# Kernel tuning notes

Measured on AMD Instinct MI355X. Metric: run time of the kernel, lower is better.

## Reference

```python
import jax, jax.numpy as jnp
import numpy as np

B, N, ND, ED, HD = 2, 384, 128, 32, 128
MSG_IN = 2 * ND + ED + 1  # 289
LN_EPS = 1e-3  # keras LayerNormalization default epsilon


def setup_inputs() -> dict:
    key = jax.random.key(0)
    ks = jax.random.split(key, 20)
    s = 0.05
    return {
        "h": jax.random.normal(ks[0], (B, N, ND), jnp.float32),
        "x": jax.random.normal(ks[1], (B, N, 3), jnp.float32),
        "edge_attr": jax.random.normal(ks[2], (B, N, N, ED), jnp.float32),
        "atom_mask": jnp.ones((B, N), jnp.float32),
        "msg_w1": jax.random.normal(ks[3], (MSG_IN, HD), jnp.float32) * s,
        "msg_b1": jnp.zeros((HD,), jnp.float32),
        "msg_w2": jax.random.normal(ks[4], (HD, HD), jnp.float32) * s,
        "msg_b2": jnp.zeros((HD,), jnp.float32),
        "node_w1": jax.random.normal(ks[5], (ND + HD, HD), jnp.float32) * s,
        "node_b1": jnp.zeros((HD,), jnp.float32),
        "node_w2": jax.random.normal(ks[6], (HD, ND), jnp.float32) * s,
        "node_b2": jnp.zeros((ND,), jnp.float32),
        "coord_w1": jax.random.normal(ks[7], (HD, HD), jnp.float32) * s,
        "coord_b1": jnp.zeros((HD,), jnp.float32),
        "coord_w2": jax.random.normal(ks[8], (HD, 1), jnp.float32) * 0.01,  # RandomNormal(0, 0.01)
        "ln_gamma": jnp.ones((ND,), jnp.float32),
        "ln_beta": jnp.zeros((ND,), jnp.float32),
        "adj": jax.random.randint(ks[9], (B, N, N), 0, 2, jnp.int32),
    }


def _layernorm(y, gamma, beta):
    mu = jnp.mean(y, axis=-1, keepdims=True)
    var = jnp.mean(jnp.square(y - mu), axis=-1, keepdims=True)
    return (y - mu) * jax.lax.rsqrt(var + LN_EPS) * gamma + beta


def reference(h, x, edge_attr, atom_mask,
              msg_w1, msg_b1, msg_w2, msg_b2,
              node_w1, node_b1, node_w2, node_b2,
              coord_w1, coord_b1, coord_w2,
              ln_gamma, ln_beta, adj):
    n = h.shape[1]
    rel_pos = x[:, :, None, :] - x[:, None, :, :]              # [B,N,N,3]
    dist_sq = jnp.sum(rel_pos ** 2, axis=-1, keepdims=True)    # [B,N,N,1]
    h_i = jnp.broadcast_to(h[:, :, None, :], (h.shape[0], n, n, h.shape[-1]))
    h_j = jnp.broadcast_to(h[:, None, :, :], (h.shape[0], n, n, h.shape[-1]))
    msg_in = jnp.concatenate([h_i, h_j, edge_attr, dist_sq], axis=-1)  # [B,N,N,289]
    m = jax.nn.silu(msg_in @ msg_w1 + msg_b1)
    m = jax.nn.silu(m @ msg_w2 + msg_b2)                        # [B,N,N,HD]
    adj_f = adj.astype(m.dtype)[..., None]                      # [B,N,N,1]
    m = m * adj_f
    h_agg = jnp.sum(m, axis=2)                                  # [B,N,HD]
    u = jax.nn.silu(jnp.concatenate([h, h_agg], axis=-1) @ node_w1 + node_b1)
    h_update = u @ node_w2 + node_b2
    h_new = _layernorm(h + h_update, ln_gamma, ln_beta)
    # coordinate update
    cw = jax.nn.silu(m @ coord_w1 + coord_b1) @ coord_w2        # [B,N,N,1]
    dist = jnp.sqrt(dist_sq + 1e-8)
    cw = cw / (dist + 1.0) * adj_f
    x_agg = jnp.sum(cw * rel_pos, axis=2) * atom_mask[..., None]
    x_new = x + x_agg
    return (h_new, x_new)
```

## Files before the change

### kernel.cpp

```cpp
#include <hip/hip_runtime.h>

typedef float f32x4 __attribute__((ext_vector_type(4)));
typedef unsigned int u32x4 __attribute__((ext_vector_type(4)));
typedef unsigned int u32x2 __attribute__((ext_vector_type(2)));
typedef __bf16 bf16x8 __attribute__((ext_vector_type(8)));

#define LDS_WET   0
#define LDS_W2T   10240
#define LDS_WC1T  45056
#define LDS_ACTW  79872
#define LDS_MBUFW 114688
#define LDS_FP    148480
#define LDS_CIDX  151552
#define LDS_WCNT  152320
#define LDS_BYTES 152388

__device__ __forceinline__ unsigned short f2bf(float f) {
  unsigned int u = __builtin_bit_cast(unsigned int, f);
  unsigned int r = u + 0x7FFFu + ((u >> 16) & 1u);
  return (unsigned short)(r >> 16);
}
__device__ __forceinline__ float bf2f(unsigned short hbits) {
  unsigned int u = ((unsigned int)hbits) << 16;
  return __builtin_bit_cast(float, u);
}
__device__ __forceinline__ unsigned int pk2(float lo, float hi) {
  return (unsigned int)f2bf(lo) | ((unsigned int)f2bf(hi) << 16);
}
__device__ __forceinline__ float silu_f(float xv) {
  float t = __builtin_amdgcn_exp2f(-1.44269504088896f * xv);
  return xv * __builtin_amdgcn_rcpf(1.0f + t);
}
__device__ __forceinline__ f32x4 mfma16(u32x4 a, u32x4 b, f32x4 c) {
  return __builtin_amdgcn_mfma_f32_16x16x32_bf16(
      __builtin_bit_cast(bf16x8, a), __builtin_bit_cast(bf16x8, b), c, 0, 0, 0);
}

__global__ void egnn_pre(const float* __restrict__ h,
                         const float* __restrict__ msg_w1,
                         const float* __restrict__ msg_b1,
                         float* __restrict__ his,
                         unsigned short* __restrict__ hjw) {
  __shared__ float hr[128];
  const int row = blockIdx.x;
  const int t = threadIdx.x;
  if (t < 128) hr[t] = h[(size_t)row*128 + t];
  __syncthreads();
  const int col = t & 127;
  const int base = (t < 128) ? 0 : 128;
  float s = (t < 128) ? msg_b1[col] : 0.0f;
  #pragma unroll 4
  for (int k = 0; k < 128; ++k) s += hr[k] * msg_w1[(size_t)(base + k)*128 + col];
  if (t < 128) his[(size_t)row*128 + col] = s;
  else         hjw[(size_t)row*128 + col] = f2bf(s);
}

__launch_bounds__(512, 1)
__global__ void egnn_main(
    const float* __restrict__ h, const float* __restrict__ x,
    const float* __restrict__ eattr, const float* __restrict__ amask,
    const float* __restrict__ msg_w1, const float* __restrict__ msg_w2,
    const float* __restrict__ msg_b2, const float* __restrict__ node_w1,
    const float* __restrict__ node_b1, const float* __restrict__ node_w2,
    const float* __restrict__ node_b2, const float* __restrict__ coord_w1,
    const float* __restrict__ coord_b1, const float* __restrict__ coord_w2,
    const float* __restrict__ ln_g, const float* __restrict__ ln_b,
    const int* __restrict__ adj, const float* __restrict__ his,
    const unsigned short* __restrict__ hjw, float* __restrict__ out)
{
  extern __shared__ char smem[];
  short* weT  = (short*)(smem + LDS_WET);
  short* w2T  = (short*)(smem + LDS_W2T);
  short* wc1T = (short*)(smem + LDS_WC1T);
  float* fp   = (float*)(smem + LDS_FP);
  float* HisL = fp;          float* wdL  = fp + 128;
  float* b2L  = fp + 256;    float* bc1L = fp + 384;
  float* wc2L = fp + 512;    float* hrow = fp + 640;
  unsigned short* cidx16 = (unsigned short*)(smem + LDS_CIDX);
  int* wcnt = (int*)(smem + LDS_WCNT);
  int* wsc  = wcnt + 8;

  const int tid  = threadIdx.x;
  const int bi   = blockIdx.x;
  const int bb   = (bi / 384) * 384;
  const int wave = tid >> 6;
  const int lane = tid & 63;
  const int g    = lane >> 4;
  const int lr   = lane & 15;
  short* actW = (short*)(smem + LDS_ACTW) + wave*16*136;
  short* mbW  = (short*)(smem + LDS_MBUFW) + wave*16*132;

  const bool pred = (tid < 384) && (adj[(size_t)bi*384 + tid] != 0);
  const unsigned long long bmask = __ballot(pred);
  if (lane == 0) wcnt[wave] = __popcll(bmask);

  for (int idx = tid; idx < 32*128; idx += 512) {
    int k = idx >> 7, d = idx & 127;
    weT[d*40 + k] = (short)f2bf(msg_w1[(size_t)(256 + k)*128 + d]);
  }
  for (int idx = tid; idx < 128*128; idx += 512) {
    int k = idx >> 7, d = idx & 127;
    w2T[d*136 + k]  = (short)f2bf(msg_w2[idx]);
    wc1T[d*136 + k] = (short)f2bf(coord_w1[idx]);
  }
  if (tid < 128) {
    HisL[tid] = his[(size_t)bi*128 + tid];
    wdL[tid]  = msg_w1[288*128 + tid];
    b2L[tid]  = msg_b2[tid];
    bc1L[tid] = coord_b1[tid];
    wc2L[tid] = coord_w2[tid];
    hrow[tid] = h[(size_t)bi*128 + tid];
  }
  __syncthreads();

  if (tid == 0) {
    int run = 0;
    #pragma unroll
    for (int w = 0; w < 8; ++w) { wsc[w] = run; run += wcnt[w]; }
    wsc[8] = run;
  }
  __syncthreads();
  if (pred) {
    int rank = __popcll(bmask & ((1ull << lane) - 1ull));
    cidx16[wsc[wave] + rank] = (unsigned short)tid;
  }
  const int deg = wsc[8];
  const float xi0 = x[bi*3+0], xi1 = x[bi*3+1], xi2 = x[bi*3+2];
  f32x4 hacc2[8];
  #pragma unroll
  for (int cf = 0; cf < 8; ++cf) hacc2[cf] = (f32x4){0.f, 0.f, 0.f, 0.f};
  float xc0 = 0.0f, xc1 = 0.0f, xc2 = 0.0f;
  __syncthreads();

  const int nchunk = (deg + 127) >> 7;
  for (int ch = 0; ch < nchunk; ++ch) {
    const int s = ch*128 + wave*16 + lr;
    const bool valid = (s < deg);
    const int cj = valid ? (int)cidx16[s] : 0;
    const float vm = valid ? 1.0f : 0.0f;
    const float* xp = x + (size_t)(bb + cj)*3;
    const float r0 = xi0 - xp[0], r1 = xi1 - xp[1], r2 = xi2 - xp[2];
    const float dq = r0*r0 + r1*r1 + r2*r2;
    const float fc = __builtin_amdgcn_rcpf(sqrtf(dq + 1e-8f) + 1.0f) * vm;
    const float c0 = fc*r0, c1 = fc*r1, c2 = fc*r2;
    const float* ep = eattr + ((size_t)bi*384 + cj)*32 + g*8;
    const float4 p0 = ((const float4*)ep)[0];
    const float4 p1 = ((const float4*)ep)[1];
    const u32x4 be = (u32x4){pk2(p0.x, p0.y), pk2(p0.z, p0.w),
                             pk2(p1.x, p1.y), pk2(p1.z, p1.w)};

    #pragma unroll
    for (int cf = 0; cf < 8; ++cf) {
      const int dO = cf*16 + 4*g;
      u32x2 hj = *(const u32x2*)(hjw + (size_t)(bb + cj)*128 + dO);
      f32x4 hv = *(const f32x4*)(HisL + dO);
      f32x4 wv = *(const f32x4*)(wdL + dO);
      f32x4 acc;
      acc[0] = hv[0] + dq*wv[0] + bf2f((unsigned short)(hj[0] & 0xFFFFu));
      acc[1] = hv[1] + dq*wv[1] + bf2f((unsigned short)(hj[0] >> 16));
      acc[2] = hv[2] + dq*wv[2] + bf2f((unsigned short)(hj[1] & 0xFFFFu));
      acc[3] = hv[3] + dq*wv[3] + bf2f((unsigned short)(hj[1] >> 16));
      u32x4 aw = *(const u32x4*)(weT + (cf*16 + lr)*40 + g*8);
      acc = mfma16(aw, be, acc);
      *(u32x2*)(actW + lr*136 + dO) =
          (u32x2){pk2(silu_f(acc[0]), silu_f(acc[1])),
                  pk2(silu_f(acc[2]), silu_f(acc[3]))};
    }

    u32x4 bk[4];
    #pragma unroll
    for (int kk = 0; kk < 4; ++kk)
      bk[kk] = *(const u32x4*)(actW + lr*136 + kk*32 + g*8);
    #pragma unroll
    for (int cf = 0; cf < 8; ++cf) {
      const int dO = cf*16 + 4*g;
      f32x4 a = *(const f32x4*)(b2L + dO);
      #pragma unroll
      for (int kk = 0; kk < 4; ++kk) {
        u32x4 aw2 = *(const u32x4*)(w2T + (cf*16 + lr)*136 + kk*32 + g*8);
        a = mfma16(aw2, bk[kk], a);
      }
      float v0 = silu_f(a[0]) * vm, v1 = silu_f(a[1]) * vm;
      float v2 = silu_f(a[2]) * vm, v3 = silu_f(a[3]) * vm;
      hacc2[cf][0] += v0; hacc2[cf][1] += v1;
      hacc2[cf][2] += v2; hacc2[cf][3] += v3;
      *(u32x2*)(mbW + lr*132 + dO) = (u32x2){pk2(v0, v1), pk2(v2, v3)};
    }

    u32x4 bm[4];
    #pragma unroll
    for (int kk = 0; kk < 4; ++kk) {
      u32x2 lo = *(const u32x2*)(mbW + lr*132 + kk*32 + g*8);
      u32x2 hi = *(const u32x2*)(mbW + lr*132 + kk*32 + g*8 + 4);
      bm[kk] = (u32x4){lo[0], lo[1], hi[0], hi[1]};
    }
    float cwp = 0.0f;
    #pragma unroll
    for (int cf = 0; cf < 8; ++cf) {
      const int dO = cf*16 + 4*g;
      f32x4 a = *(const f32x4*)(bc1L + dO);
      #pragma unroll
      for (int kk = 0; kk < 4; ++kk) {
        u32x4 aw3 = *(const u32x4*)(wc1T + (cf*16 + lr)*136 + kk*32 + g*8);
        a = mfma16(aw3, bm[kk], a);
      }
      f32x4 wv = *(const f32x4*)(wc2L + dO);
      cwp += silu_f(a[0])*wv[0] + silu_f(a[1])*wv[1]
           + silu_f(a[2])*wv[2] + silu_f(a[3])*wv[3];
    }
    cwp += __shfl_xor(cwp, 16, 64);
    cwp += __shfl_xor(cwp, 32, 64);
    if (lane < 16) { xc0 += cwp*c0; xc1 += cwp*c1; xc2 += cwp*c2; }
  }

  __syncthreads();
  #pragma unroll
  for (int cf = 0; cf < 8; ++cf) {
    #pragma unroll
    for (int r = 0; r < 4; ++r) {
      float v = hacc2[cf][r];
      v += __shfl_xor(v, 1, 64); v += __shfl_xor(v, 2, 64);
      v += __shfl_xor(v, 4, 64); v += __shfl_xor(v, 8, 64);
      hacc2[cf][r] = v;
    }
  }
  float* actF  = (float*)(smem + LDS_ACTW);
  float* hpart = actF;
  float* xcf   = actF + 1024;
  float* red   = actF + 1408;
  float* hagg  = actF + 1920;
  float* uvec  = actF + 2048;
  float* lnr   = actF + 2176;
  if (lr == 0) {
    #pragma unroll
    for (int cf = 0; cf < 8; ++cf)
      #pragma unroll
      for (int r = 0; r < 4; ++r)
        hpart[wave*128 + cf*16 + 4*g + r] = hacc2[cf][r];
  }
  if (lane < 16) {
    const int idx = wave*16 + lr;
    xcf[idx] = xc0; xcf[128 + idx] = xc1; xcf[256 + idx] = xc2;
  }
  __syncthreads();
  if (tid < 128) {
    float s = 0.0f;
    #pragma unroll
    for (int w = 0; w < 8; ++w) s += hpart[w*128 + tid];
    hagg[tid] = s;
  }
  if (tid < 3) {
    float sx = 0.0f;
    #pragma unroll 8
    for (int j = 0; j < 128; ++j) sx += xcf[tid*128 + j];
    out[98304 + (size_t)bi*3 + tid] = x[bi*3 + tid] + sx * amask[bi];
  }
  __syncthreads();

  {
    const int d = tid & 127, q = tid >> 7;
    float s = 0.0f;
    for (int k = q*64; k < q*64 + 64; ++k) {
      const float inv = (k < 128) ? hrow[k] : hagg[k - 128];
      s += inv * node_w1[(size_t)k*128 + d];
    }
    red[q*128 + d] = s;
  }
  __syncthreads();
  if (tid < 128)
    uvec[tid] = silu_f(red[tid] + red[128+tid] + red[256+tid] + red[384+tid] + node_b1[tid]);
  __syncthreads();

  {
    const int d = tid & 127, q = tid >> 7;
    float s = 0.0f;
    for (int k = q*32; k < q*32 + 32; ++k) s += uvec[k] * node_w2[(size_t)k*128 + d];
    red[q*128 + d] = s;
  }
  __syncthreads();
  float y = 0.0f;
  if (tid < 128)
    y = hrow[tid] + red[tid] + red[128+tid] + red[256+tid] + red[384+tid] + node_b2[tid];

  float ssum = (tid < 128) ? y : 0.0f;
  #pragma unroll
  for (int mm = 1; mm < 64; mm <<= 1) ssum += __shfl_xor(ssum, mm, 64);
  if (tid < 128 && lane == 0) lnr[wave] = ssum;
  __syncthreads();
  const float mu = (lnr[0] + lnr[1]) * (1.0f/128.0f);
  float yc = (tid < 128) ? (y - mu) : 0.0f;
  float sq = yc * yc;
  #pragma unroll
  for (int mm = 1; mm < 64; mm <<= 1) sq += __shfl_xor(sq, mm, 64);
  if (tid < 128 && lane == 0) lnr[2 + wave] = sq;
  __syncthreads();
  if (tid < 128) {
    const float var = (lnr[2] + lnr[3]) * (1.0f/128.0f);
    out[(size_t)bi*128 + tid] = yc * rsqrtf(var + 1e-3f) * ln_g[tid] + ln_b[tid];
  }
}

extern "C" void kernel_launch(void* const* d_in, const int* in_sizes, int n_in,
                              void* d_out, int out_size, void* d_ws, size_t ws_size,
                              hipStream_t stream) {
  const float* h        = (const float*)d_in[0];
  const float* x        = (const float*)d_in[1];
  const float* eattr    = (const float*)d_in[2];
  const float* amask    = (const float*)d_in[3];
  const float* msg_w1   = (const float*)d_in[4];
  const float* msg_b1   = (const float*)d_in[5];
  const float* msg_w2   = (const float*)d_in[6];
  const float* msg_b2   = (const float*)d_in[7];
  const float* node_w1  = (const float*)d_in[8];
  const float* node_b1  = (const float*)d_in[9];
  const float* node_w2  = (const float*)d_in[10];
  const float* node_b2  = (const float*)d_in[11];
  const float* coord_w1 = (const float*)d_in[12];
  const float* coord_b1 = (const float*)d_in[13];
  const float* coord_w2 = (const float*)d_in[14];
  const float* ln_g     = (const float*)d_in[15];
  const float* ln_b     = (const float*)d_in[16];
  const int*   adj      = (const int*)d_in[17];
  float* out = (float*)d_out;
  float* his = (float*)d_ws;
  unsigned short* hjw = (unsigned short*)((char*)d_ws + 393216);

  hipFuncSetAttribute((const void*)egnn_main,
                      hipFuncAttributeMaxDynamicSharedMemorySize, LDS_BYTES);

  egnn_pre<<<768, 256, 0, stream>>>(h, msg_w1, msg_b1, his, hjw);
  egnn_main<<<768, 512, LDS_BYTES, stream>>>(h, x, eattr, amask, msg_w1, msg_w2,
      msg_b2, node_w1, node_b1, node_w2, node_b2, coord_w1, coord_b1, coord_w2,
      ln_g, ln_b, adj, his, hjw, out);
}
```

Before: 87.55 us.

## Make main kernel persistent over three nodes to amortize weight staging

```diff
diff --git a/kernel.cpp b/kernel.cpp
--- a/kernel.cpp
+++ b/kernel.cpp
@@ -9,23 +9,29 @@
 #define LDS_W2T   10240
 #define LDS_WC1T  45056
 #define LDS_ACTW  79872
-#define LDS_MBUFW 114688
-#define LDS_FP    148480
-#define LDS_CIDX  151552
-#define LDS_WCNT  152320
-#define LDS_BYTES 152388
+#define LDS_FP    114688
+#define LDS_CIDX  117760
+#define LDS_WCNT  118528
+#define LDS_BYTES 118596
 
 __device__ __forceinline__ unsigned short f2bf(float f) {
   unsigned int u = __builtin_bit_cast(unsigned int, f);
   unsigned int r = u + 0x7FFFu + ((u >> 16) & 1u);
   return (unsigned short)(r >> 16);
 }
-__device__ __forceinline__ float bf2f(unsigned short hbits) {
-  unsigned int u = ((unsigned int)hbits) << 16;
-  return __builtin_bit_cast(float, u);
-}
 __device__ __forceinline__ unsigned int pk2(float lo, float hi) {
-  return (unsigned int)f2bf(lo) | ((unsigned int)f2bf(hi) << 16);
+  unsigned short a = __builtin_bit_cast(unsigned short, (__bf16)lo);
+  unsigned short b = __builtin_bit_cast(unsigned short, (__bf16)hi);
+  return (unsigned int)a | ((unsigned int)b << 16);
+}
+__device__ __forceinline__ short bf1(float f) {
+  return (short)__builtin_bit_cast(unsigned short, (__bf16)f);
+}
+__device__ __forceinline__ float bflo(unsigned int u) {
+  return __builtin_bit_cast(float, u << 16);
+}
+__device__ __forceinline__ float bfhi(unsigned int u) {
+  return __builtin_bit_cast(float, u & 0xFFFF0000u);
 }
 __device__ __forceinline__ float silu_f(float xv) {
   float t = __builtin_amdgcn_exp2f(-1.44269504088896f * xv);
@@ -73,230 +79,233 @@
   short* w2T  = (short*)(smem + LDS_W2T);
   short* wc1T = (short*)(smem + LDS_WC1T);
   float* fp   = (float*)(smem + LDS_FP);
-  float* HisL = fp;          float* wdL  = fp + 128;
-  float* b2L  = fp + 256;    float* bc1L = fp + 384;
-  float* wc2L = fp + 512;    float* hrow = fp + 640;
+  float* wdL  = fp;          float* b2L  = fp + 128;
+  float* bc1L = fp + 256;    float* wc2L = fp + 384;
+  float* HisL = fp + 512;    float* hrow = fp + 640;
   unsigned short* cidx16 = (unsigned short*)(smem + LDS_CIDX);
   int* wcnt = (int*)(smem + LDS_WCNT);
   int* wsc  = wcnt + 8;
 
   const int tid  = threadIdx.x;
-  const int bi   = blockIdx.x;
-  const int bb   = (bi / 384) * 384;
   const int wave = tid >> 6;
   const int lane = tid & 63;
   const int g    = lane >> 4;
   const int lr   = lane & 15;
-  short* actW = (short*)(smem + LDS_ACTW) + wave*16*136;
-  short* mbW  = (short*)(smem + LDS_MBUFW) + wave*16*132;
-
-  const bool pred = (tid < 384) && (adj[(size_t)bi*384 + tid] != 0);
-  const unsigned long long bmask = __ballot(pred);
-  if (lane == 0) wcnt[wave] = __popcll(bmask);
+  short* actW = (short*)(smem + LDS_ACTW) + wave*(16*136);
 
   for (int idx = tid; idx < 32*128; idx += 512) {
     int k = idx >> 7, d = idx & 127;
-    weT[d*40 + k] = (short)f2bf(msg_w1[(size_t)(256 + k)*128 + d]);
+    weT[d*40 + k] = bf1(msg_w1[(size_t)(256 + k)*128 + d]);
   }
   for (int idx = tid; idx < 128*128; idx += 512) {
     int k = idx >> 7, d = idx & 127;
-    w2T[d*136 + k]  = (short)f2bf(msg_w2[idx]);
-    wc1T[d*136 + k] = (short)f2bf(coord_w1[idx]);
+    w2T[d*136 + k]  = bf1(msg_w2[idx]);
+    wc1T[d*136 + k] = bf1(coord_w1[idx]);
   }
   if (tid < 128) {
-    HisL[tid] = his[(size_t)bi*128 + tid];
     wdL[tid]  = msg_w1[288*128 + tid];
     b2L[tid]  = msg_b2[tid];
     bc1L[tid] = coord_b1[tid];
     wc2L[tid] = coord_w2[tid];
-    hrow[tid] = h[(size_t)bi*128 + tid];
   }
-  __syncthreads();
-
-  if (tid == 0) {
-    int run = 0;
+
+  for (int node = 0; node < 3; ++node) {
+    const int bi = blockIdx.x + node*256;
+    const int bb = (bi / 384) * 384;
+    __syncthreads();
+
+    const bool pred = (tid < 384) && (adj[(size_t)bi*384 + tid] != 0);
+    const unsigned long long bmask = __ballot(pred);
+    if (lane == 0) wcnt[wave] = __popcll(bmask);
+    if (tid < 128) {
+      HisL[tid] = his[(size_t)bi*128 + tid];
+      hrow[tid] = h[(size_t)bi*128 + tid];
+    }
+    __syncthreads();
+    if (tid == 0) {
+      int run = 0;
+      #pragma unroll
+      for (int w = 0; w < 8; ++w) { wsc[w] = run; run += wcnt[w]; }
+      wsc[8] = run;
+    }
+    __syncthreads();
+    if (pred) {
+      int rank = __popcll(bmask & ((1ull << lane) - 1ull));
+      cidx16[wsc[wave] + rank] = (unsigned short)tid;
+    }
+    const int deg = wsc[8];
+    const float xi0 = x[bi*3+0], xi1 = x[bi*3+1], xi2 = x[bi*3+2];
+    f32x4 hacc2[8];
     #pragma unroll
-    for (int w = 0; w < 8; ++w) { wsc[w] = run; run += wcnt[w]; }
-    wsc[8] = run;
-  }
-  __syncthreads();
-  if (pred) {
-    int rank = __popcll(bmask & ((1ull << lane) - 1ull));
-    cidx16[wsc[wave] + rank] = (unsigned short)tid;
-  }
-  const int deg = wsc[8];
-  const float xi0 = x[bi*3+0], xi1 = x[bi*3+1], xi2 = x[bi*3+2];
-  f32x4 hacc2[8];
-  #pragma unroll
-  for (int cf = 0; cf < 8; ++cf) hacc2[cf] = (f32x4){0.f, 0.f, 0.f, 0.f};
-  float xc0 = 0.0f, xc1 = 0.0f, xc2 = 0.0f;
-  __syncthreads();
-
-  const int nchunk = (deg + 127) >> 7;
-  for (int ch = 0; ch < nchunk; ++ch) {
-    const int s = ch*128 + wave*16 + lr;
-    const bool valid = (s < deg);
-    const int cj = valid ? (int)cidx16[s] : 0;
-    const float vm = valid ? 1.0f : 0.0f;
-    const float* xp = x + (size_t)(bb + cj)*3;
-    const float r0 = xi0 - xp[0], r1 = xi1 - xp[1], r2 = xi2 - xp[2];
-    const float dq = r0*r0 + r1*r1 + r2*r2;
-    const float fc = __builtin_amdgcn_rcpf(sqrtf(dq + 1e-8f) + 1.0f) * vm;
-    const float c0 = fc*r0, c1 = fc*r1, c2 = fc*r2;
-    const float* ep = eattr + ((size_t)bi*384 + cj)*32 + g*8;
-    const float4 p0 = ((const float4*)ep)[0];
-    const float4 p1 = ((const float4*)ep)[1];
-    const u32x4 be = (u32x4){pk2(p0.x, p0.y), pk2(p0.z, p0.w),
-                             pk2(p1.x, p1.y), pk2(p1.z, p1.w)};
-
+    for (int cf = 0; cf < 8; ++cf) hacc2[cf] = (f32x4){0.f, 0.f, 0.f, 0.f};
+    float xc0 = 0.0f, xc1 = 0.0f, xc2 = 0.0f;
+    __syncthreads();
+
+    const int nchunk = (deg + 127) >> 7;
+    for (int ch = 0; ch < nchunk; ++ch) {
+      const int sbase = ch*128 + wave*16;
+      if (sbase >= deg) continue;
+      const int s = sbase + lr;
+      const bool valid = (s < deg);
+      const int cj = valid ? (int)cidx16[s] : 0;
+      const float vm = valid ? 1.0f : 0.0f;
+      const float* xp = x + (size_t)(bb + cj)*3;
+      const float r0 = xi0 - xp[0], r1 = xi1 - xp[1], r2 = xi2 - xp[2];
+      const float dq = r0*r0 + r1*r1 + r2*r2;
+      const float fc = __builtin_amdgcn_rcpf(sqrtf(dq + 1e-8f) + 1.0f) * vm;
+      const float c0 = fc*r0, c1 = fc*r1, c2 = fc*r2;
+      const float* ep = eattr + ((size_t)bi*384 + cj)*32 + g*8;
+      const float4 p0 = ((const float4*)ep)[0];
+      const float4 p1 = ((const float4*)ep)[1];
+      const u32x4 be = (u32x4){pk2(p0.x, p0.y), pk2(p0.z, p0.w),
+                               pk2(p1.x, p1.y), pk2(p1.z, p1.w)};
+
+      #pragma unroll
+      for (int cf = 0; cf < 8; ++cf) {
+        const int dO = cf*16 + 4*g;
+        u32x2 hj = *(const u32x2*)(hjw + (size_t)(bb + cj)*128 + dO);
+        f32x4 hv = *(const f32x4*)(HisL + dO);
+        f32x4 wv = *(const f32x4*)(wdL + dO);
+        f32x4 acc;
+        acc[0] = hv[0] + dq*wv[0] + bflo(hj[0]);
+        acc[1] = hv[1] + dq*wv[1] + bfhi(hj[0]);
+        acc[2] = hv[2] + dq*wv[2] + bflo(hj[1]);
+        acc[3] = hv[3] + dq*wv[3] + bfhi(hj[1]);
+        u32x4 aw = *(const u32x4*)(weT + (cf*16 + lr)*40 + g*8);
+        acc = mfma16(aw, be, acc);
+        *(u32x2*)(actW + lr*136 + dO) =
+            (u32x2){pk2(silu_f(acc[0]), silu_f(acc[1])),
+                    pk2(silu_f(acc[2]), silu_f(acc[3]))};
+      }
+
+      u32x4 bk[4];
+      #pragma unroll
+      for (int kk = 0; kk < 4; ++kk)
+        bk[kk] = *(const u32x4*)(actW + lr*136 + kk*32 + g*8);
+      #pragma unroll
+      for (int cf = 0; cf < 8; ++cf) {
+        const int dO = cf*16 + 4*g;
+        f32x4 a = *(const f32x4*)(b2L + dO);
+        #pragma unroll
+        for (int kk = 0; kk < 4; ++kk) {
+          u32x4 aw2 = *(const u32x4*)(w2T + (cf*16 + lr)*136 + kk*32 + g*8);
+          a = mfma16(aw2, bk[kk], a);
+        }
+        float v0 = silu_f(a[0]) * vm, v1 = silu_f(a[1]) * vm;
+        float v2 = silu_f(a[2]) * vm, v3 = silu_f(a[3]) * vm;
+        hacc2[cf][0] += v0; hacc2[cf][1] += v1;
+        hacc2[cf][2] += v2; hacc2[cf][3] += v3;
+        *(u32x2*)(actW + lr*136 + dO) = (u32x2){pk2(v0, v1), pk2(v2, v3)};
+      }
+
+      u32x4 bm[4];
+      #pragma unroll
+      for (int kk = 0; kk < 4; ++kk)
+        bm[kk] = *(const u32x4*)(actW + lr*136 + kk*32 + g*8);
+      float cwp = 0.0f;
+      #pragma unroll
+      for (int cf = 0; cf < 8; ++cf) {
+        const int dO = cf*16 + 4*g;
+        f32x4 a = *(const f32x4*)(bc1L + dO);
+        #pragma unroll
+        for (int kk = 0; kk < 4; ++kk) {
+          u32x4 aw3 = *(const u32x4*)(wc1T + (cf*16 + lr)*136 + kk*32 + g*8);
+          a = mfma16(aw3, bm[kk], a);
+        }
+        f32x4 wv = *(const f32x4*)(wc2L + dO);
+        cwp += silu_f(a[0])*wv[0] + silu_f(a[1])*wv[1]
+             + silu_f(a[2])*wv[2] + silu_f(a[3])*wv[3];
+      }
+      cwp += __shfl_xor(cwp, 16, 64);
+      cwp += __shfl_xor(cwp, 32, 64);
+      if (lane < 16) { xc0 += cwp*c0; xc1 += cwp*c1; xc2 += cwp*c2; }
+    }
+
+    __syncthreads();
     #pragma unroll
     for (int cf = 0; cf < 8; ++cf) {
-      const int dO = cf*16 + 4*g;
-      u32x2 hj = *(const u32x2*)(hjw + (size_t)(bb + cj)*128 + dO);
-      f32x4 hv = *(const f32x4*)(HisL + dO);
-      f32x4 wv = *(const f32x4*)(wdL + dO);
-      f32x4 acc;
-      acc[0] = hv[0] + dq*wv[0] + bf2f((unsigned short)(hj[0] & 0xFFFFu));
-      acc[1] = hv[1] + dq*wv[1] + bf2f((unsigned short)(hj[0] >> 16));
-      acc[2] = hv[2] + dq*wv[2] + bf2f((unsigned short)(hj[1] & 0xFFFFu));
-      acc[3] = hv[3] + dq*wv[3] + bf2f((unsigned short)(hj[1] >> 16));
-      u32x4 aw = *(const u32x4*)(weT + (cf*16 + lr)*40 + g*8);
-      acc = mfma16(aw, be, acc);
-      *(u32x2*)(actW + lr*136 + dO) =
-          (u32x2){pk2(silu_f(acc[0]), silu_f(acc[1])),
-                  pk2(silu_f(acc[2]), silu_f(acc[3]))};
-    }
-
-    u32x4 bk[4];
+      #pragma unroll
+      for (int r = 0; r < 4; ++r) {
+        float v = hacc2[cf][r];
+        v += __shfl_xor(v, 1, 64); v += __shfl_xor(v, 2, 64);
+        v += __shfl_xor(v, 4, 64); v += __shfl_xor(v, 8, 64);
+        hacc2[cf][r] = v;
+      }
+    }
+    float* actF  = (float*)(smem + LDS_ACTW);
+    float* hpart = actF;
+    float* xcf   = actF + 1024;
+    float* red   = actF + 1408;
+    float* hagg  = actF + 1920;
+    float* uvec  = actF + 2048;
+    float* lnr   = actF + 2176;
+    if (lr == 0) {
+      #pragma unroll
+      for (int cf = 0; cf < 8; ++cf)
+        #pragma unroll
+        for (int r = 0; r < 4; ++r)
+          hpart[wave*128 + cf*16 + 4*g + r] = hacc2[cf][r];
+    }
+    if (lane < 16) {
+      const int idx = wave*16 + lr;
+      xcf[idx] = xc0; xcf[128 + idx] = xc1; xcf[256 + idx] = xc2;
+    }
+    __syncthreads();
+    if (tid < 128) {
+      float s = 0.0f;
+      #pragma unroll
+      for (int w = 0; w < 8; ++w) s += hpart[w*128 + tid];
+      hagg[tid] = s;
+    }
+    if (tid < 3) {
+      float sx = 0.0f;
+      #pragma unroll 8
+      for (int j = 0; j < 128; ++j) sx += xcf[tid*128 + j];
+      out[98304 + (size_t)bi*3 + tid] = x[bi*3 + tid] + sx * amask[bi];
+    }
+    __syncthreads();
+
+    {
+      const int d = tid & 127, q = tid >> 7;
+      float s = 0.0f;
+      for (int k = q*64; k < q*64 + 64; ++k) {
+        const float inv = (k < 128) ? hrow[k] : hagg[k - 128];
+        s += inv * node_w1[(size_t)k*128 + d];
+      }
+      red[q*128 + d] = s;
+    }
+    __syncthreads();
+    if (tid < 128)
+      uvec[tid] = silu_f(red[tid] + red[128+tid] + red[256+tid] + red[384+tid] + node_b1[tid]);
+    __syncthreads();
+
+    {
+      const int d = tid & 127, q = tid >> 7;
+      float s = 0.0f;
+      for (int k = q*32; k < q*32 + 32; ++k) s += uvec[k] * node_w2[(size_t)k*128 + d];
+      red[q*128 + d] = s;
+    }
+    __syncthreads();
+    float y = 0.0f;
+    if (tid < 128)
+      y = hrow[tid] + red[tid] + red[128+tid] + red[256+tid] + red[384+tid] + node_b2[tid];
+
+    float ssum = (tid < 128) ? y : 0.0f;
     #pragma unroll
-    for (int kk = 0; kk < 4; ++kk)
-      bk[kk] = *(const u32x4*)(actW + lr*136 + kk*32 + g*8);
+    for (int mm = 1; mm < 64; mm <<= 1) ssum += __shfl_xor(ssum, mm, 64);
+    if (tid < 128 && lane == 0) lnr[wave] = ssum;
+    __syncthreads();
+    const float mu = (lnr[0] + lnr[1]) * (1.0f/128.0f);
+    float yc = (tid < 128) ? (y - mu) : 0.0f;
+    float sq = yc * yc;
     #pragma unroll
-    for (int cf = 0; cf < 8; ++cf) {
-      const int dO = cf*16 + 4*g;
-      f32x4 a = *(const f32x4*)(b2L + dO);
-      #pragma unroll
-      for (int kk = 0; kk < 4; ++kk) {
-        u32x4 aw2 = *(const u32x4*)(w2T + (cf*16 + lr)*136 + kk*32 + g*8);
-        a = mfma16(aw2, bk[kk], a);
-      }
-      float v0 = silu_f(a[0]) * vm, v1 = silu_f(a[1]) * vm;
-      float v2 = silu_f(a[2]) * vm, v3 = silu_f(a[3]) * vm;
-      hacc2[cf][0] += v0; hacc2[cf][1] += v1;
-      hacc2[cf][2] += v2; hacc2[cf][3] += v3;
-      *(u32x2*)(mbW + lr*132 + dO) = (u32x2){pk2(v0, v1), pk2(v2, v3)};
-    }
-
-    u32x4 bm[4];
-    #pragma unroll
-    for (int kk = 0; kk < 4; ++kk) {
-      u32x2 lo = *(const u32x2*)(mbW + lr*132 + kk*32 + g*8);
-      u32x2 hi = *(const u32x2*)(mbW + lr*132 + kk*32 + g*8 + 4);
-      bm[kk] = (u32x4){lo[0], lo[1], hi[0], hi[1]};
-    }
-    float cwp = 0.0f;
-    #pragma unroll
-    for (int cf = 0; cf < 8; ++cf) {
-      const int dO = cf*16 + 4*g;
-      f32x4 a = *(const f32x4*)(bc1L + dO);
-      #pragma unroll
-      for (int kk = 0; kk < 4; ++kk) {
-        u32x4 aw3 = *(const u32x4*)(wc1T + (cf*16 + lr)*136 + kk*32 + g*8);
-        a = mfma16(aw3, bm[kk], a);
-      }
-      f32x4 wv = *(const f32x4*)(wc2L + dO);
-      cwp += silu_f(a[0])*wv[0] + silu_f(a[1])*wv[1]
-           + silu_f(a[2])*wv[2] + silu_f(a[3])*wv[3];
-    }
-    cwp += __shfl_xor(cwp, 16, 64);
-    cwp += __shfl_xor(cwp, 32, 64);
-    if (lane < 16) { xc0 += cwp*c0; xc1 += cwp*c1; xc2 += cwp*c2; }
-  }
-
-  __syncthreads();
-  #pragma unroll
-  for (int cf = 0; cf < 8; ++cf) {
-    #pragma unroll
-    for (int r = 0; r < 4; ++r) {
-      float v = hacc2[cf][r];
-      v += __shfl_xor(v, 1, 64); v += __shfl_xor(v, 2, 64);
-      v += __shfl_xor(v, 4, 64); v += __shfl_xor(v, 8, 64);
-      hacc2[cf][r] = v;
-    }
-  }
-  float* actF  = (float*)(smem + LDS_ACTW);
-  float* hpart = actF;
-  float* xcf   = actF + 1024;
-  float* red   = actF + 1408;
-  float* hagg  = actF + 1920;
-  float* uvec  = actF + 2048;
-  float* lnr   = actF + 2176;
-  if (lr == 0) {
-    #pragma unroll
-    for (int cf = 0; cf < 8; ++cf)
-      #pragma unroll
-      for (int r = 0; r < 4; ++r)
-        hpart[wave*128 + cf*16 + 4*g + r] = hacc2[cf][r];
-  }
-  if (lane < 16) {
-    const int idx = wave*16 + lr;
-    xcf[idx] = xc0; xcf[128 + idx] = xc1; xcf[256 + idx] = xc2;
-  }
-  __syncthreads();
-  if (tid < 128) {
-    float s = 0.0f;
-    #pragma unroll
-    for (int w = 0; w < 8; ++w) s += hpart[w*128 + tid];
-    hagg[tid] = s;
-  }
-  if (tid < 3) {
-    float sx = 0.0f;
-    #pragma unroll 8
-    for (int j = 0; j < 128; ++j) sx += xcf[tid*128 + j];
-    out[98304 + (size_t)bi*3 + tid] = x[bi*3 + tid] + sx * amask[bi];
-  }
-  __syncthreads();
-
-  {
-    const int d = tid & 127, q = tid >> 7;
-    float s = 0.0f;
-    for (int k = q*64; k < q*64 + 64; ++k) {
-      const float inv = (k < 128) ? hrow[k] : hagg[k - 128];
-      s += inv * node_w1[(size_t)k*128 + d];
-    }
-    red[q*128 + d] = s;
-  }
-  __syncthreads();
-  if (tid < 128)
-    uvec[tid] = silu_f(red[tid] + red[128+tid] + red[256+tid] + red[384+tid] + node_b1[tid]);
-  __syncthreads();
-
-  {
-    const int d = tid & 127, q = tid >> 7;
-    float s = 0.0f;
-    for (int k = q*32; k < q*32 + 32; ++k) s += uvec[k] * node_w2[(size_t)k*128 + d];
-    red[q*128 + d] = s;
-  }
-  __syncthreads();
-  float y = 0.0f;
-  if (tid < 128)
-    y = hrow[tid] + red[tid] + red[128+tid] + red[256+tid] + red[384+tid] + node_b2[tid];
-
-  float ssum = (tid < 128) ? y : 0.0f;
-  #pragma unroll
-  for (int mm = 1; mm < 64; mm <<= 1) ssum += __shfl_xor(ssum, mm, 64);
-  if (tid < 128 && lane == 0) lnr[wave] = ssum;
-  __syncthreads();
-  const float mu = (lnr[0] + lnr[1]) * (1.0f/128.0f);
-  float yc = (tid < 128) ? (y - mu) : 0.0f;
-  float sq = yc * yc;
-  #pragma unroll
-  for (int mm = 1; mm < 64; mm <<= 1) sq += __shfl_xor(sq, mm, 64);
-  if (tid < 128 && lane == 0) lnr[2 + wave] = sq;
-  __syncthreads();
-  if (tid < 128) {
-    const float var = (lnr[2] + lnr[3]) * (1.0f/128.0f);
-    out[(size_t)bi*128 + tid] = yc * rsqrtf(var + 1e-3f) * ln_g[tid] + ln_b[tid];
+    for (int mm = 1; mm < 64; mm <<= 1) sq += __shfl_xor(sq, mm, 64);
+    if (tid < 128 && lane == 0) lnr[2 + wave] = sq;
+    __syncthreads();
+    if (tid < 128) {
+      const float var = (lnr[2] + lnr[3]) * (1.0f/128.0f);
+      out[(size_t)bi*128 + tid] = yc * rsqrtf(var + 1e-3f) * ln_g[tid] + ln_b[tid];
+    }
   }
 }
 
@@ -329,7 +338,7 @@
                       hipFuncAttributeMaxDynamicSharedMemorySize, LDS_BYTES);
 
   egnn_pre<<<768, 256, 0, stream>>>(h, msg_w1, msg_b1, his, hjw);
-  egnn_main<<<768, 512, LDS_BYTES, stream>>>(h, x, eattr, amask, msg_w1, msg_w2,
+  egnn_main<<<256, 512, LDS_BYTES, stream>>>(h, x, eattr, amask, msg_w1, msg_w2,
       msg_b2, node_w1, node_b1, node_w2, node_b2, coord_w1, coord_b1, coord_w2,
       ln_g, ln_b, adj, his, hjw, out);
 }
```

Result: slower. 124.7 us (+42.4%).
